# Kernel optimization log

Hardware: AMD Instinct MI355X
Metric: run time of the kernel (lower is better)

Reference implementation:

```python
import jax, jax.numpy as jnp
import numpy as np

K = 128   # per-head dim == input dim
H = 8     # heads
B = 2
T = 2048


def setup_inputs() -> dict:
    key = jax.random.key(0)
    ks = jax.random.split(key, 6)
    s_in = 1.0 / np.sqrt(K)
    s_out = 1.0 / np.sqrt(K * H)
    return {
        "x": jax.random.normal(ks[0], (B, T, K), dtype=jnp.float32),
        # Linear weights stored as (in, out); torch Linear init ~ U(-1/sqrt(in), 1/sqrt(in))
        "Wq": jax.random.uniform(ks[1], (K, K * H), jnp.float32, -s_in, s_in),
        "Wk": jax.random.uniform(ks[2], (K, K * H), jnp.float32, -s_in, s_in),
        "Wv": jax.random.uniform(ks[3], (K, K * H), jnp.float32, -s_in, s_in),
        "Wo": jax.random.uniform(ks[4], (K * H, K), jnp.float32, -s_out, s_out),
        "bo": jax.random.uniform(ks[5], (K,), jnp.float32, -s_out, s_out),
    }


def reference(x, Wq, Wk, Wv, Wo, bo):
    b, t, k = x.shape
    h = H
    scale = k ** 0.25
    # projections -> [b, t, h, k]
    q = (x @ Wq).reshape(b, t, h, k) / scale
    ke = (x @ Wk).reshape(b, t, h, k) / scale
    v = (x @ Wv).reshape(b, t, h, k)
    # scores: [b, h, t, t]
    scores = jnp.einsum('bihk,bjhk->bhij', q, ke)
    # causal mask: positions j > i get -inf (diagonal kept)
    causal = jnp.tril(jnp.ones((t, t), dtype=bool))
    scores = jnp.where(causal[None, None], scores, -jnp.inf)
    p = jax.nn.softmax(scores, axis=-1)
    out = jnp.einsum('bhij,bjhk->bihk', p, v).reshape(b, t, h * k)
    return out @ Wo + bo
```

## Files before the change

kernel.cpp:

```cpp
#include <hip/hip_runtime.h>

typedef __bf16 bf16;
typedef __bf16 bf16x4 __attribute__((ext_vector_type(4)));
typedef __bf16 bf16x8 __attribute__((ext_vector_type(8)));
typedef float f32x4 __attribute__((ext_vector_type(4)));
typedef float f32x16 __attribute__((ext_vector_type(16)));
typedef int i32x4 __attribute__((ext_vector_type(4)));

#define MFMA16(a, b, c) __builtin_amdgcn_mfma_f32_16x16x32_bf16((a), (b), (c), 0, 0, 0)
#define MFMA32(a, b, c) __builtin_amdgcn_mfma_f32_32x32x16_bf16((a), (b), (c), 0, 0, 0)

__device__ __forceinline__ int swz16(int r, int c) { return (c ^ (r & 15)); }

__device__ __forceinline__ int cvt_pk_bf16(float lo, float hi) {
  int r;
  asm("v_cvt_pk_bf16_f32 %0, %1, %2" : "=v"(r) : "v"(lo), "v"(hi));
  return r;
}

__global__ __launch_bounds__(256) void trW_kernel(
    const float* __restrict__ Wq, const float* __restrict__ Wk,
    const float* __restrict__ Wv, const float* __restrict__ Wo,
    bf16* __restrict__ outbase) {
  __shared__ bf16 tile[32][33];
  const int z = blockIdx.z;
  const float* ib = (z == 0) ? Wq : (z == 1) ? Wk : (z == 2) ? Wv : Wo;
  bf16* ob = outbase + (size_t)z * 131072;
  const int R = (z < 3) ? 128 : 1024;
  const int C = (z < 3) ? 1024 : 128;
  int r0 = (z < 3) ? blockIdx.y * 32 : blockIdx.x * 32;
  int c0 = (z < 3) ? blockIdx.x * 32 : blockIdx.y * 32;
  int tx = threadIdx.x & 31, ty = threadIdx.x >> 5;
#pragma unroll
  for (int i = 0; i < 4; ++i) {
    int r = ty + i * 8;
    tile[r][tx] = (bf16)ib[(size_t)(r0 + r) * C + (c0 + tx)];
  }
  __syncthreads();
#pragma unroll
  for (int i = 0; i < 4; ++i) {
    int r = ty + i * 8;
    ob[(size_t)(c0 + r) * R + (r0 + tx)] = tile[tx][r];
  }
}

__global__ __launch_bounds__(256) void proj_gemm(
    const float* __restrict__ x, const bf16* __restrict__ Wqt,
    const bf16* __restrict__ Wkt, const bf16* __restrict__ Wvt,
    bf16* __restrict__ Qf, bf16* __restrict__ Kf, bf16* __restrict__ Vf) {
  __shared__ __align__(16) bf16 As[128 * 128];
  __shared__ __align__(16) bf16 Bs[128 * 128];
  const int mt = blockIdx.x;
  const int nt = blockIdx.y;
  const int matid = nt >> 3, h = nt & 7;
  const bf16* W = (matid == 0) ? Wqt : (matid == 1) ? Wkt : Wvt;
  const int tid = threadIdx.x;
  const bf16* sb = W + (size_t)h * 128 * 128;
#pragma unroll
  for (int i = 0; i < 8; ++i) {
    int c = tid + i * 256;
    int r = c >> 4, cc = c & 15;
    const f32x4* p = (const f32x4*)(x + (size_t)(mt * 128 + r) * 128 + cc * 8);
    f32x4 a = p[0], b = p[1];
    bf16x8 o;
#pragma unroll
    for (int j = 0; j < 4; ++j) { o[j] = (bf16)a[j]; o[4 + j] = (bf16)b[j]; }
    *(bf16x8*)&As[r * 128 + swz16(r, cc) * 8] = o;
  }
#pragma unroll
  for (int i = 0; i < 8; ++i) {
    int c = tid + i * 256;
    int r = c >> 4, cc = c & 15;
    *(bf16x8*)&Bs[r * 128 + swz16(r, cc) * 8] = *(const bf16x8*)(sb + (size_t)r * 128 + cc * 8);
  }
  __syncthreads();
  const int wave = tid >> 6, lane = tid & 63;
  const int wr = (wave >> 1) * 64, wc = (wave & 1) * 64;
  const int lr = lane & 15, lkb = lane >> 4;
  const f32x4 FZ = {0.f, 0.f, 0.f, 0.f};
  f32x4 acc[4][4];
#pragma unroll
  for (int mf = 0; mf < 4; ++mf)
#pragma unroll
    for (int nf = 0; nf < 4; ++nf) acc[mf][nf] = FZ;
  const bool qk = (matid < 2);
#pragma unroll
  for (int ks = 0; ks < 4; ++ks) {
    bf16x8 a[4], b[4];
#pragma unroll
    for (int mf = 0; mf < 4; ++mf) {
      int r = wr + mf * 16 + lr;
      a[mf] = *(const bf16x8*)&As[r * 128 + swz16(r, ks * 4 + lkb) * 8];
    }
#pragma unroll
    for (int nf = 0; nf < 4; ++nf) {
      int r = wc + nf * 16 + lr;
      b[nf] = *(const bf16x8*)&Bs[r * 128 + swz16(r, ks * 4 + lkb) * 8];
    }
    if (qk) {
#pragma unroll
      for (int mf = 0; mf < 4; ++mf)
#pragma unroll
        for (int nf = 0; nf < 4; ++nf) acc[mf][nf] = MFMA16(b[nf], a[mf], acc[mf][nf]);
    } else {
#pragma unroll
      for (int mf = 0; mf < 4; ++mf)
#pragma unroll
        for (int nf = 0; nf < 4; ++nf) acc[mf][nf] = MFMA16(a[mf], b[nf], acc[mf][nf]);
    }
  }
  const int rb = lkb * 4;
  if (qk) {
    bf16* Out = (matid == 0) ? Qf : Kf;
#pragma unroll
    for (int mf = 0; mf < 4; ++mf)
#pragma unroll
      for (int nf = 0; nf < 4; ++nf) {
        int m = mt * 128 + wr + mf * 16 + lr;
        int d0 = wc + nf * 16 + rb;
        int bb = m >> 11, t = m & 2047;
        bf16x4 vv;
#pragma unroll
        for (int r = 0; r < 4; ++r) vv[r] = (bf16)acc[mf][nf][r];
        size_t e = (size_t)(bb * 8 + h) * 262144
                 + (size_t)(((t >> 5) * 8 + (d0 >> 4)) * 512 + ((d0 >> 3) & 1) * 256
                            + (t & 31) * 8 + (d0 & 7));
        *(bf16x4*)(Out + e) = vv;
      }
  } else {
#pragma unroll
    for (int mf = 0; mf < 4; ++mf)
#pragma unroll
      for (int nf = 0; nf < 4; ++nf) {
        int d = wc + nf * 16 + lr;
        int m0 = mt * 128 + wr + mf * 16 + rb;
        int bb = m0 >> 11, t0 = m0 & 2047;
        bf16x4 vv;
#pragma unroll
        for (int r = 0; r < 4; ++r) vv[r] = (bf16)acc[mf][nf][r];
        size_t e = (size_t)(bb * 8 + h) * 262144
                 + (size_t)((d >> 5) * 65536 + (t0 >> 4) * 512 + ((t0 >> 3) & 1) * 256
                            + (d & 31) * 8 + (t0 & 7));
        *(bf16x4*)(Vf + e) = vv;
      }
  }
}

__global__ __launch_bounds__(256, 3) void attn_kernel(
    bf16* __restrict__ Qf, const bf16* __restrict__ Kf, const bf16* __restrict__ Vf) {
  __shared__ float Om0[128 * 32];
  __shared__ float Om1[128 * 32];
  __shared__ float L0m[32], L0l[32], L1m[32], L1l[32];
  const int bid = blockIdx.x;
  const int bh = bid & 15;
  const int qt = 63 - (bid >> 4);
  const int tid = threadIdx.x;
  const int w = tid >> 6, lane = tid & 63;
  const int lq = lane & 31, hi = lane >> 5;
  const int lo = hi * 256 + lq * 8;
  const bf16* Qh = Qf + (size_t)bh * 262144;
  const bf16* Kh = Kf + (size_t)bh * 262144;
  const bf16* Vh = Vf + (size_t)bh * 262144;
  const float SCL = 0.12751744f;

  const int nT = (qt >> 1) + 1;
  const int base = nT >> 2, rem = nT & 3;
  const int cnt = base + (w < rem ? 1 : 0);
  const int tb = w * base + (w < rem ? w : rem);

  bf16x8 qf[8];
#pragma unroll
  for (int ks = 0; ks < 8; ++ks)
    qf[ks] = *(const bf16x8*)(Qh + qt * 4096 + ks * 512 + lo);

  float mrun = -__builtin_inff(), lrun = 0.f;
  f32x16 O[4];
#pragma unroll
  for (int dt = 0; dt < 4; ++dt)
#pragma unroll
    for (int r = 0; r < 16; ++r) O[dt][r] = 0.f;

  for (int it = 0; it < cnt; ++it) {
    const int kvt = tb + it;
    const int kv0 = kvt * 64;
    const bf16* kbase = Kh + kvt * 8192 + lo;
    bf16x8 ka[8], kb[8];
#pragma unroll
    for (int i = 0; i < 8; ++i) ka[i] = *(const bf16x8*)(kbase + i * 512);
#pragma unroll
    for (int i = 0; i < 8; ++i) kb[i] = *(const bf16x8*)(kbase + 4096 + i * 512);
    f32x16 p0, p1;
#pragma unroll
    for (int r = 0; r < 16; ++r) { p0[r] = 0.f; p1[r] = 0.f; }
    __builtin_amdgcn_s_setprio(1);
#pragma unroll
    for (int ks = 0; ks < 8; ++ks) p0 = MFMA32(ka[ks], qf[ks], p0);
#pragma unroll
    for (int ks = 0; ks < 8; ++ks) p1 = MFMA32(kb[ks], qf[ks], p1);
    __builtin_amdgcn_s_setprio(0);
    const bf16* vbase = Vh + kvt * 2048 + lo;
    bf16x8 va[8];
#pragma unroll
    for (int i = 0; i < 8; ++i)
      va[i] = *(const bf16x8*)(vbase + (i >> 2) * 65536 + (i & 3) * 512);
    if (kvt == (qt >> 1)) {
      const int qg = qt * 32 + lq;
#pragma unroll
      for (int r = 0; r < 16; ++r) {
        int kvr = kv0 + (r & 3) + 8 * (r >> 2) + 4 * hi;
        if (kvr > qg) p0[r] = -__builtin_inff();
        if (kvr + 32 > qg) p1[r] = -__builtin_inff();
      }
    }
    float m0 = fmaxf(p0[0], p1[0]);
    float m1_ = fmaxf(p0[1], p1[1]);
    float m2 = fmaxf(p0[2], p1[2]);
    float m3 = fmaxf(p0[3], p1[3]);
#pragma unroll
    for (int r = 4; r < 16; r += 4) {
      m0 = fmaxf(m0, fmaxf(p0[r], p1[r]));
      m1_ = fmaxf(m1_, fmaxf(p0[r + 1], p1[r + 1]));
      m2 = fmaxf(m2, fmaxf(p0[r + 2], p1[r + 2]));
      m3 = fmaxf(m3, fmaxf(p0[r + 3], p1[r + 3]));
    }
    float pm = fmaxf(fmaxf(m0, m1_), fmaxf(m2, m3));
    pm = fmaxf(pm, __shfl_xor(pm, 32, 64));
    float pmS = pm * SCL;
    if (!__all(pmS <= mrun + 8.f)) {
      float mnew = fmaxf(mrun, pmS);
      float alpha = exp2f(mrun - mnew);
      mrun = mnew;
      lrun *= alpha;
#pragma unroll
      for (int dt = 0; dt < 4; ++dt)
#pragma unroll
        for (int r = 0; r < 16; ++r) O[dt][r] *= alpha;
    }
    float s0 = 0.f, s1 = 0.f, s2 = 0.f, s3 = 0.f;
#pragma unroll
    for (int r = 0; r < 16; r += 4) {
      float a0_ = exp2f(__builtin_fmaf(p0[r], SCL, -mrun));
      float a1_ = exp2f(__builtin_fmaf(p0[r + 1], SCL, -mrun));
      float a2_ = exp2f(__builtin_fmaf(p0[r + 2], SCL, -mrun));
      float a3_ = exp2f(__builtin_fmaf(p0[r + 3], SCL, -mrun));
      float b0_ = exp2f(__builtin_fmaf(p1[r], SCL, -mrun));
      float b1_ = exp2f(__builtin_fmaf(p1[r + 1], SCL, -mrun));
      float b2_ = exp2f(__builtin_fmaf(p1[r + 2], SCL, -mrun));
      float b3_ = exp2f(__builtin_fmaf(p1[r + 3], SCL, -mrun));
      p0[r] = a0_; p0[r + 1] = a1_; p0[r + 2] = a2_; p0[r + 3] = a3_;
      p1[r] = b0_; p1[r + 1] = b1_; p1[r + 2] = b2_; p1[r + 3] = b3_;
      s0 += a0_ + b0_; s1 += a1_ + b1_; s2 += a2_ + b2_; s3 += a3_ + b3_;
    }
    float ps = (s0 + s1) + (s2 + s3);
    ps += __shfl_xor(ps, 32, 64);
    lrun += ps;
    int wd[16];
#pragma unroll
    for (int i = 0; i < 8; ++i) wd[i] = cvt_pk_bf16(p0[2 * i], p0[2 * i + 1]);
#pragma unroll
    for (int i = 0; i < 8; ++i) wd[8 + i] = cvt_pk_bf16(p1[2 * i], p1[2 * i + 1]);
    bf16x8 pa[4];
#pragma unroll
    for (int t4 = 0; t4 < 4; ++t4) {
      int b0 = t4 * 4;
      int e0 = __shfl_xor(wd[b0 + 0], 32, 64);
      int e1 = __shfl_xor(wd[b0 + 1], 32, 64);
      int e2 = __shfl_xor(wd[b0 + 2], 32, 64);
      int e3 = __shfl_xor(wd[b0 + 3], 32, 64);
      i32x4 f;
      f[0] = hi ? e2 : wd[b0 + 0];
      f[1] = hi ? e3 : wd[b0 + 1];
      f[2] = hi ? wd[b0 + 2] : e0;
      f[3] = hi ? wd[b0 + 3] : e1;
      pa[t4] = __builtin_bit_cast(bf16x8, f);
    }
    bf16x8 vb[8];
#pragma unroll
    for (int i = 0; i < 8; ++i)
      vb[i] = *(const bf16x8*)(vbase + 131072 + (i >> 2) * 65536 + (i & 3) * 512);
    __builtin_amdgcn_s_setprio(1);
#pragma unroll
    for (int dt = 0; dt < 2; ++dt) {
      O[dt] = MFMA32(va[dt * 4 + 0], pa[0], O[dt]);
      O[dt] = MFMA32(va[dt * 4 + 1], pa[1], O[dt]);
      O[dt] = MFMA32(va[dt * 4 + 2], pa[2], O[dt]);
      O[dt] = MFMA32(va[dt * 4 + 3], pa[3], O[dt]);
    }
#pragma unroll
    for (int dt = 0; dt < 2; ++dt) {
      O[2 + dt] = MFMA32(vb[dt * 4 + 0], pa[0], O[2 + dt]);
      O[2 + dt] = MFMA32(vb[dt * 4 + 1], pa[1], O[2 + dt]);
      O[2 + dt] = MFMA32(vb[dt * 4 + 2], pa[2], O[2 + dt]);
      O[2 + dt] = MFMA32(vb[dt * 4 + 3], pa[3], O[2 + dt]);
    }
    __builtin_amdgcn_s_setprio(0);
  }

  auto STORE = [&](float* Om, float* Lm, float* Ll) {
#pragma unroll
    for (int dt = 0; dt < 4; ++dt)
#pragma unroll
      for (int r = 0; r < 16; ++r)
        Om[(dt * 32 + (r & 3) + 8 * (r >> 2) + 4 * hi) * 32 + lq] = O[dt][r];
    if (!hi) { Lm[lq] = mrun; Ll[lq] = lrun; }
  };
  auto MERGE = [&](const float* Om, const float* Lm, const float* Ll) {
    float m1 = Lm[lq], l1 = Ll[lq];
    float mF = fmaxf(mrun, m1);
    float a0 = (mrun < -3.0e38f) ? 0.f : exp2f(mrun - mF);
    float a1 = (m1 < -3.0e38f) ? 0.f : exp2f(m1 - mF);
    lrun = lrun * a0 + l1 * a1;
#pragma unroll
    for (int dt = 0; dt < 4; ++dt)
#pragma unroll
      for (int r = 0; r < 16; ++r)
        O[dt][r] = O[dt][r] * a0 +
                   Om[(dt * 32 + (r & 3) + 8 * (r >> 2) + 4 * hi) * 32 + lq] * a1;
    mrun = mF;
  };

  if (w == 1) STORE(Om0, L0m, L0l);
  if (w == 3) STORE(Om1, L1m, L1l);
  __syncthreads();
  if (w == 0) MERGE(Om0, L0m, L0l);
  if (w == 2) MERGE(Om1, L1m, L1l);
  __syncthreads();
  if (w == 2) STORE(Om0, L0m, L0l);
  __syncthreads();
  if (w == 0) {
    MERGE(Om0, L0m, L0l);
    float inv = 1.f / lrun;
    bf16* qw = Qf + (size_t)bh * 262144 + qt * 4096 + lq * 8 + 4 * hi;
#pragma unroll
    for (int dt = 0; dt < 4; ++dt) {
#pragma unroll
      for (int rq = 0; rq < 4; ++rq) {
        bf16x4 vv;
#pragma unroll
        for (int jj = 0; jj < 4; ++jj) {
          int r = rq * 4 + jj;
          vv[jj] = (bf16)(O[dt][r] * inv);
        }
        *(bf16x4*)(qw + (dt * 2 + (rq >> 1)) * 512 + (rq & 1) * 256) = vv;
      }
    }
  }
}

__global__ __launch_bounds__(256) void outproj_kernel(
    const bf16* __restrict__ AO, const bf16* __restrict__ Wot,
    const float* __restrict__ bo, float* __restrict__ out) {
  __shared__ __align__(16) bf16 As[16 * 128];
  __shared__ __align__(16) bf16 Bs[128 * 128];
  const f32x4 FZ = {0.f, 0.f, 0.f, 0.f};
  const int mt = blockIdx.x;
  const int tid = threadIdx.x, wave = tid >> 6, lane = tid & 63;
  const int lr = lane & 15, lkb = lane >> 4, rb = lkb * 4;
  const int wc = wave * 32;
  f32x4 acc[2];
  acc[0] = FZ; acc[1] = FZ;
  for (int kt = 0; kt < 8; ++kt) {
    __syncthreads();
    {
      int r = tid >> 4, cc = tid & 15;
      int m = mt * 16 + r, bb = m >> 11, t = m & 2047;
      const bf16* src = AO + (size_t)(bb * 8 + kt) * 262144
          + ((t >> 5) * 8 + (cc >> 1)) * 512 + (cc & 1) * 256 + (t & 31) * 8;
      *(bf16x8*)&As[r * 128 + swz16(r, cc) * 8] = *(const bf16x8*)src;
    }
#pragma unroll
    for (int i = 0; i < 8; ++i) {
      int c = tid + i * 256;
      int r = c >> 4, cc = c & 15;
      *(bf16x8*)&Bs[r * 128 + swz16(r, cc) * 8] =
          *(const bf16x8*)(Wot + (size_t)r * 1024 + kt * 128 + cc * 8);
    }
    __syncthreads();
#pragma unroll
    for (int ks = 0; ks < 4; ++ks) {
      bf16x8 a = *(const bf16x8*)&As[lr * 128 + swz16(lr, ks * 4 + lkb) * 8];
#pragma unroll
      for (int nf = 0; nf < 2; ++nf) {
        int r = wc + nf * 16 + lr;
        bf16x8 b = *(const bf16x8*)&Bs[r * 128 + swz16(r, ks * 4 + lkb) * 8];
        acc[nf] = MFMA16(a, b, acc[nf]);
      }
    }
  }
#pragma unroll
  for (int nf = 0; nf < 2; ++nf)
#pragma unroll
    for (int r = 0; r < 4; ++r) {
      int m = mt * 16 + rb + r;
      int n = wc + nf * 16 + lr;
      out[(size_t)m * 128 + n] = acc[nf][r] + bo[n];
    }
}

extern "C" void kernel_launch(void* const* d_in, const int* in_sizes, int n_in,
                              void* d_out, int out_size, void* d_ws, size_t ws_size,
                              hipStream_t stream) {
  (void)in_sizes; (void)n_in; (void)out_size; (void)ws_size;
  const float* x  = (const float*)d_in[0];
  const float* Wq = (const float*)d_in[1];
  const float* Wk = (const float*)d_in[2];
  const float* Wv = (const float*)d_in[3];
  const float* Wo = (const float*)d_in[4];
  const float* bo = (const float*)d_in[5];
  float* out = (float*)d_out;

  bf16* ws  = (bf16*)d_ws;
  bf16* Wqt = ws;
  bf16* Wkt = Wqt + 131072;
  bf16* Wvt = Wkt + 131072;
  bf16* Wot = Wvt + 131072;
  bf16* Qf  = Wot + 131072;
  bf16* Kf  = Qf + 4194304;
  bf16* Vf  = Kf + 4194304;

  trW_kernel<<<dim3(32, 4, 4), 256, 0, stream>>>(Wq, Wk, Wv, Wo, Wqt);
  proj_gemm<<<dim3(32, 24, 1), 256, 0, stream>>>(x, Wqt, Wkt, Wvt, Qf, Kf, Vf);
  attn_kernel<<<dim3(1024, 1, 1), 256, 0, stream>>>(Qf, Kf, Vf);
  outproj_kernel<<<dim3(256, 1, 1), 256, 0, stream>>>(Qf, Wot, bo, out);
}
```

Baseline: 160.7 us.

## Pair causal q-tiles per block with 512-thread blocks for balanced attention work

Restructures the attention kernel so each 512-thread block handles two adjacent 32-row query tiles, with two groups of four waves, and processes two phases pairing query tile pr with 31-pr. This balances causal work per block and shrinks the grid from 1024 to 256 blocks, each with a 66.5KB dynamic-shared-memory merge buffer. It also shares K/V tiles between the two query groups in cache. The 256-block grid and large LDS footprint limit occupancy to about one block per CU, and the extra barriers between phases add synchronisation cost.

```diff
diff --git a/kernel.cpp b/kernel.cpp
--- a/kernel.cpp
+++ b/kernel.cpp
@@ -146,16 +146,16 @@
   }
 }
 
-__global__ __launch_bounds__(256, 3) void attn_kernel(
+__global__ __launch_bounds__(512) void attn_kernel(
     bf16* __restrict__ Qf, const bf16* __restrict__ Kf, const bf16* __restrict__ Vf) {
-  __shared__ float Om0[128 * 32];
-  __shared__ float Om1[128 * 32];
-  __shared__ float L0m[32], L0l[32], L1m[32], L1l[32];
+  extern __shared__ char smem[];
   const int bid = blockIdx.x;
   const int bh = bid & 15;
-  const int qt = 63 - (bid >> 4);
+  const int pr = bid >> 4;
   const int tid = threadIdx.x;
   const int w = tid >> 6, lane = tid & 63;
+  const int qs = w >> 2;
+  const int k4 = w & 3;
   const int lq = lane & 31, hi = lane >> 5;
   const int lo = hi * 256 + lq * 8;
   const bf16* Qh = Qf + (size_t)bh * 262144;
@@ -163,185 +163,202 @@
   const bf16* Vh = Vf + (size_t)bh * 262144;
   const float SCL = 0.12751744f;
 
-  const int nT = (qt >> 1) + 1;
-  const int base = nT >> 2, rem = nT & 3;
-  const int cnt = base + (w < rem ? 1 : 0);
-  const int tb = w * base + (w < rem ? w : rem);
-
-  bf16x8 qf[8];
-#pragma unroll
-  for (int ks = 0; ks < 8; ++ks)
-    qf[ks] = *(const bf16x8*)(Qh + qt * 4096 + ks * 512 + lo);
-
-  float mrun = -__builtin_inff(), lrun = 0.f;
-  f32x16 O[4];
-#pragma unroll
-  for (int dt = 0; dt < 4; ++dt)
-#pragma unroll
-    for (int r = 0; r < 16; ++r) O[dt][r] = 0.f;
-
-  for (int it = 0; it < cnt; ++it) {
-    const int kvt = tb + it;
-    const int kv0 = kvt * 64;
-    const bf16* kbase = Kh + kvt * 8192 + lo;
-    bf16x8 ka[8], kb[8];
-#pragma unroll
-    for (int i = 0; i < 8; ++i) ka[i] = *(const bf16x8*)(kbase + i * 512);
-#pragma unroll
-    for (int i = 0; i < 8; ++i) kb[i] = *(const bf16x8*)(kbase + 4096 + i * 512);
-    f32x16 p0, p1;
-#pragma unroll
-    for (int r = 0; r < 16; ++r) { p0[r] = 0.f; p1[r] = 0.f; }
-    __builtin_amdgcn_s_setprio(1);
-#pragma unroll
-    for (int ks = 0; ks < 8; ++ks) p0 = MFMA32(ka[ks], qf[ks], p0);
-#pragma unroll
-    for (int ks = 0; ks < 8; ++ks) p1 = MFMA32(kb[ks], qf[ks], p1);
-    __builtin_amdgcn_s_setprio(0);
-    const bf16* vbase = Vh + kvt * 2048 + lo;
-    bf16x8 va[8];
-#pragma unroll
-    for (int i = 0; i < 8; ++i)
-      va[i] = *(const bf16x8*)(vbase + (i >> 2) * 65536 + (i & 3) * 512);
-    if (kvt == (qt >> 1)) {
-      const int qg = qt * 32 + lq;
-#pragma unroll
-      for (int r = 0; r < 16; ++r) {
-        int kvr = kv0 + (r & 3) + 8 * (r >> 2) + 4 * hi;
-        if (kvr > qg) p0[r] = -__builtin_inff();
-        if (kvr + 32 > qg) p1[r] = -__builtin_inff();
-      }
-    }
-    float m0 = fmaxf(p0[0], p1[0]);
-    float m1_ = fmaxf(p0[1], p1[1]);
-    float m2 = fmaxf(p0[2], p1[2]);
-    float m3 = fmaxf(p0[3], p1[3]);
-#pragma unroll
-    for (int r = 4; r < 16; r += 4) {
-      m0 = fmaxf(m0, fmaxf(p0[r], p1[r]));
-      m1_ = fmaxf(m1_, fmaxf(p0[r + 1], p1[r + 1]));
-      m2 = fmaxf(m2, fmaxf(p0[r + 2], p1[r + 2]));
-      m3 = fmaxf(m3, fmaxf(p0[r + 3], p1[r + 3]));
-    }
-    float pm = fmaxf(fmaxf(m0, m1_), fmaxf(m2, m3));
-    pm = fmaxf(pm, __shfl_xor(pm, 32, 64));
-    float pmS = pm * SCL;
-    if (!__all(pmS <= mrun + 8.f)) {
-      float mnew = fmaxf(mrun, pmS);
-      float alpha = exp2f(mrun - mnew);
-      mrun = mnew;
-      lrun *= alpha;
+  float* OmB[4];
+  float* LmB[4];
+  float* LlB[4];
+#pragma unroll
+  for (int b = 0; b < 4; ++b) {
+    OmB[b] = (float*)(smem + b * 16384);
+    LmB[b] = (float*)(smem + 65536 + b * 128);
+    LlB[b] = (float*)(smem + 66048 + b * 128);
+  }
+
+  for (int ph = 0; ph < 2; ++ph) {
+    const int qt64 = ph ? (31 - pr) : pr;
+    const int nT = qt64 + 1;
+    const int qblk = qt64 * 2 + qs;
+    const int k4e = ph ? (3 - k4) : k4;
+    const int base = nT >> 2, rem = nT & 3;
+    const int cnt = base + (k4e < rem ? 1 : 0);
+    const int tb = k4e * base + (k4e < rem ? k4e : rem);
+
+    bf16x8 qf[8];
+#pragma unroll
+    for (int ks = 0; ks < 8; ++ks)
+      qf[ks] = *(const bf16x8*)(Qh + qblk * 4096 + ks * 512 + lo);
+
+    float mrun = -__builtin_inff(), lrun = 0.f;
+    f32x16 O[4];
+#pragma unroll
+    for (int dt = 0; dt < 4; ++dt)
+#pragma unroll
+      for (int r = 0; r < 16; ++r) O[dt][r] = 0.f;
+
+    for (int it = 0; it < cnt; ++it) {
+      const int kvt = tb + it;
+      const int kv0 = kvt * 64;
+      const bf16* kbase = Kh + kvt * 8192 + lo;
+      bf16x8 ka[8], kb[8];
+#pragma unroll
+      for (int i = 0; i < 8; ++i) ka[i] = *(const bf16x8*)(kbase + i * 512);
+#pragma unroll
+      for (int i = 0; i < 8; ++i) kb[i] = *(const bf16x8*)(kbase + 4096 + i * 512);
+      f32x16 p0, p1;
+#pragma unroll
+      for (int r = 0; r < 16; ++r) { p0[r] = 0.f; p1[r] = 0.f; }
+      __builtin_amdgcn_s_setprio(1);
+#pragma unroll
+      for (int ks = 0; ks < 8; ++ks) p0 = MFMA32(ka[ks], qf[ks], p0);
+#pragma unroll
+      for (int ks = 0; ks < 8; ++ks) p1 = MFMA32(kb[ks], qf[ks], p1);
+      __builtin_amdgcn_s_setprio(0);
+      const bf16* vbase = Vh + kvt * 2048 + lo;
+      bf16x8 va[8];
+#pragma unroll
+      for (int i = 0; i < 8; ++i)
+        va[i] = *(const bf16x8*)(vbase + (i >> 2) * 65536 + (i & 3) * 512);
+      if (kvt == qt64) {
+        const int qg = qblk * 32 + lq;
+#pragma unroll
+        for (int r = 0; r < 16; ++r) {
+          int kvr = kv0 + (r & 3) + 8 * (r >> 2) + 4 * hi;
+          if (kvr > qg) p0[r] = -__builtin_inff();
+          if (kvr + 32 > qg) p1[r] = -__builtin_inff();
+        }
+      }
+      float m0 = fmaxf(p0[0], p1[0]);
+      float m1_ = fmaxf(p0[1], p1[1]);
+      float m2 = fmaxf(p0[2], p1[2]);
+      float m3 = fmaxf(p0[3], p1[3]);
+#pragma unroll
+      for (int r = 4; r < 16; r += 4) {
+        m0 = fmaxf(m0, fmaxf(p0[r], p1[r]));
+        m1_ = fmaxf(m1_, fmaxf(p0[r + 1], p1[r + 1]));
+        m2 = fmaxf(m2, fmaxf(p0[r + 2], p1[r + 2]));
+        m3 = fmaxf(m3, fmaxf(p0[r + 3], p1[r + 3]));
+      }
+      float pm = fmaxf(fmaxf(m0, m1_), fmaxf(m2, m3));
+      pm = fmaxf(pm, __shfl_xor(pm, 32, 64));
+      float pmS = pm * SCL;
+      if (!__all(pmS <= mrun + 8.f)) {
+        float mnew = fmaxf(mrun, pmS);
+        float alpha = exp2f(mrun - mnew);
+        mrun = mnew;
+        lrun *= alpha;
+#pragma unroll
+        for (int dt = 0; dt < 4; ++dt)
+#pragma unroll
+          for (int r = 0; r < 16; ++r) O[dt][r] *= alpha;
+      }
+      float s0 = 0.f, s1 = 0.f, s2 = 0.f, s3 = 0.f;
+#pragma unroll
+      for (int r = 0; r < 16; r += 4) {
+        float a0_ = exp2f(__builtin_fmaf(p0[r], SCL, -mrun));
+        float a1_ = exp2f(__builtin_fmaf(p0[r + 1], SCL, -mrun));
+        float a2_ = exp2f(__builtin_fmaf(p0[r + 2], SCL, -mrun));
+        float a3_ = exp2f(__builtin_fmaf(p0[r + 3], SCL, -mrun));
+        float b0_ = exp2f(__builtin_fmaf(p1[r], SCL, -mrun));
+        float b1_ = exp2f(__builtin_fmaf(p1[r + 1], SCL, -mrun));
+        float b2_ = exp2f(__builtin_fmaf(p1[r + 2], SCL, -mrun));
+        float b3_ = exp2f(__builtin_fmaf(p1[r + 3], SCL, -mrun));
+        p0[r] = a0_; p0[r + 1] = a1_; p0[r + 2] = a2_; p0[r + 3] = a3_;
+        p1[r] = b0_; p1[r + 1] = b1_; p1[r + 2] = b2_; p1[r + 3] = b3_;
+        s0 += a0_ + b0_; s1 += a1_ + b1_; s2 += a2_ + b2_; s3 += a3_ + b3_;
+      }
+      float ps = (s0 + s1) + (s2 + s3);
+      ps += __shfl_xor(ps, 32, 64);
+      lrun += ps;
+      int wd[16];
+#pragma unroll
+      for (int i = 0; i < 8; ++i) wd[i] = cvt_pk_bf16(p0[2 * i], p0[2 * i + 1]);
+#pragma unroll
+      for (int i = 0; i < 8; ++i) wd[8 + i] = cvt_pk_bf16(p1[2 * i], p1[2 * i + 1]);
+      bf16x8 pa[4];
+#pragma unroll
+      for (int t4 = 0; t4 < 4; ++t4) {
+        int b0 = t4 * 4;
+        int e0 = __shfl_xor(wd[b0 + 0], 32, 64);
+        int e1 = __shfl_xor(wd[b0 + 1], 32, 64);
+        int e2 = __shfl_xor(wd[b0 + 2], 32, 64);
+        int e3 = __shfl_xor(wd[b0 + 3], 32, 64);
+        i32x4 f;
+        f[0] = hi ? e2 : wd[b0 + 0];
+        f[1] = hi ? e3 : wd[b0 + 1];
+        f[2] = hi ? wd[b0 + 2] : e0;
+        f[3] = hi ? wd[b0 + 3] : e1;
+        pa[t4] = __builtin_bit_cast(bf16x8, f);
+      }
+      bf16x8 vb[8];
+#pragma unroll
+      for (int i = 0; i < 8; ++i)
+        vb[i] = *(const bf16x8*)(vbase + 131072 + (i >> 2) * 65536 + (i & 3) * 512);
+      __builtin_amdgcn_s_setprio(1);
+#pragma unroll
+      for (int dt = 0; dt < 2; ++dt) {
+        O[dt] = MFMA32(va[dt * 4 + 0], pa[0], O[dt]);
+        O[dt] = MFMA32(va[dt * 4 + 1], pa[1], O[dt]);
+        O[dt] = MFMA32(va[dt * 4 + 2], pa[2], O[dt]);
+        O[dt] = MFMA32(va[dt * 4 + 3], pa[3], O[dt]);
+      }
+#pragma unroll
+      for (int dt = 0; dt < 2; ++dt) {
+        O[2 + dt] = MFMA32(vb[dt * 4 + 0], pa[0], O[2 + dt]);
+        O[2 + dt] = MFMA32(vb[dt * 4 + 1], pa[1], O[2 + dt]);
+        O[2 + dt] = MFMA32(vb[dt * 4 + 2], pa[2], O[2 + dt]);
+        O[2 + dt] = MFMA32(vb[dt * 4 + 3], pa[3], O[2 + dt]);
+      }
+      __builtin_amdgcn_s_setprio(0);
+    }
+
+    auto STORE = [&](float* Om, float* Lm, float* Ll) {
 #pragma unroll
       for (int dt = 0; dt < 4; ++dt)
 #pragma unroll
-        for (int r = 0; r < 16; ++r) O[dt][r] *= alpha;
-    }
-    float s0 = 0.f, s1 = 0.f, s2 = 0.f, s3 = 0.f;
-#pragma unroll
-    for (int r = 0; r < 16; r += 4) {
-      float a0_ = exp2f(__builtin_fmaf(p0[r], SCL, -mrun));
-      float a1_ = exp2f(__builtin_fmaf(p0[r + 1], SCL, -mrun));
-      float a2_ = exp2f(__builtin_fmaf(p0[r + 2], SCL, -mrun));
-      float a3_ = exp2f(__builtin_fmaf(p0[r + 3], SCL, -mrun));
-      float b0_ = exp2f(__builtin_fmaf(p1[r], SCL, -mrun));
-      float b1_ = exp2f(__builtin_fmaf(p1[r + 1], SCL, -mrun));
-      float b2_ = exp2f(__builtin_fmaf(p1[r + 2], SCL, -mrun));
-      float b3_ = exp2f(__builtin_fmaf(p1[r + 3], SCL, -mrun));
-      p0[r] = a0_; p0[r + 1] = a1_; p0[r + 2] = a2_; p0[r + 3] = a3_;
-      p1[r] = b0_; p1[r + 1] = b1_; p1[r + 2] = b2_; p1[r + 3] = b3_;
-      s0 += a0_ + b0_; s1 += a1_ + b1_; s2 += a2_ + b2_; s3 += a3_ + b3_;
-    }
-    float ps = (s0 + s1) + (s2 + s3);
-    ps += __shfl_xor(ps, 32, 64);
-    lrun += ps;
-    int wd[16];
-#pragma unroll
-    for (int i = 0; i < 8; ++i) wd[i] = cvt_pk_bf16(p0[2 * i], p0[2 * i + 1]);
-#pragma unroll
-    for (int i = 0; i < 8; ++i) wd[8 + i] = cvt_pk_bf16(p1[2 * i], p1[2 * i + 1]);
-    bf16x8 pa[4];
-#pragma unroll
-    for (int t4 = 0; t4 < 4; ++t4) {
-      int b0 = t4 * 4;
-      int e0 = __shfl_xor(wd[b0 + 0], 32, 64);
-      int e1 = __shfl_xor(wd[b0 + 1], 32, 64);
-      int e2 = __shfl_xor(wd[b0 + 2], 32, 64);
-      int e3 = __shfl_xor(wd[b0 + 3], 32, 64);
-      i32x4 f;
-      f[0] = hi ? e2 : wd[b0 + 0];
-      f[1] = hi ? e3 : wd[b0 + 1];
-      f[2] = hi ? wd[b0 + 2] : e0;
-      f[3] = hi ? wd[b0 + 3] : e1;
-      pa[t4] = __builtin_bit_cast(bf16x8, f);
-    }
-    bf16x8 vb[8];
-#pragma unroll
-    for (int i = 0; i < 8; ++i)
-      vb[i] = *(const bf16x8*)(vbase + 131072 + (i >> 2) * 65536 + (i & 3) * 512);
-    __builtin_amdgcn_s_setprio(1);
-#pragma unroll
-    for (int dt = 0; dt < 2; ++dt) {
-      O[dt] = MFMA32(va[dt * 4 + 0], pa[0], O[dt]);
-      O[dt] = MFMA32(va[dt * 4 + 1], pa[1], O[dt]);
-      O[dt] = MFMA32(va[dt * 4 + 2], pa[2], O[dt]);
-      O[dt] = MFMA32(va[dt * 4 + 3], pa[3], O[dt]);
-    }
-#pragma unroll
-    for (int dt = 0; dt < 2; ++dt) {
-      O[2 + dt] = MFMA32(vb[dt * 4 + 0], pa[0], O[2 + dt]);
-      O[2 + dt] = MFMA32(vb[dt * 4 + 1], pa[1], O[2 + dt]);
-      O[2 + dt] = MFMA32(vb[dt * 4 + 2], pa[2], O[2 + dt]);
-      O[2 + dt] = MFMA32(vb[dt * 4 + 3], pa[3], O[2 + dt]);
-    }
-    __builtin_amdgcn_s_setprio(0);
-  }
-
-  auto STORE = [&](float* Om, float* Lm, float* Ll) {
-#pragma unroll
-    for (int dt = 0; dt < 4; ++dt)
-#pragma unroll
-      for (int r = 0; r < 16; ++r)
-        Om[(dt * 32 + (r & 3) + 8 * (r >> 2) + 4 * hi) * 32 + lq] = O[dt][r];
-    if (!hi) { Lm[lq] = mrun; Ll[lq] = lrun; }
-  };
-  auto MERGE = [&](const float* Om, const float* Lm, const float* Ll) {
-    float m1 = Lm[lq], l1 = Ll[lq];
-    float mF = fmaxf(mrun, m1);
-    float a0 = (mrun < -3.0e38f) ? 0.f : exp2f(mrun - mF);
-    float a1 = (m1 < -3.0e38f) ? 0.f : exp2f(m1 - mF);
-    lrun = lrun * a0 + l1 * a1;
-#pragma unroll
-    for (int dt = 0; dt < 4; ++dt)
-#pragma unroll
-      for (int r = 0; r < 16; ++r)
-        O[dt][r] = O[dt][r] * a0 +
-                   Om[(dt * 32 + (r & 3) + 8 * (r >> 2) + 4 * hi) * 32 + lq] * a1;
-    mrun = mF;
-  };
-
-  if (w == 1) STORE(Om0, L0m, L0l);
-  if (w == 3) STORE(Om1, L1m, L1l);
-  __syncthreads();
-  if (w == 0) MERGE(Om0, L0m, L0l);
-  if (w == 2) MERGE(Om1, L1m, L1l);
-  __syncthreads();
-  if (w == 2) STORE(Om0, L0m, L0l);
-  __syncthreads();
-  if (w == 0) {
-    MERGE(Om0, L0m, L0l);
-    float inv = 1.f / lrun;
-    bf16* qw = Qf + (size_t)bh * 262144 + qt * 4096 + lq * 8 + 4 * hi;
-#pragma unroll
-    for (int dt = 0; dt < 4; ++dt) {
-#pragma unroll
-      for (int rq = 0; rq < 4; ++rq) {
-        bf16x4 vv;
-#pragma unroll
-        for (int jj = 0; jj < 4; ++jj) {
-          int r = rq * 4 + jj;
-          vv[jj] = (bf16)(O[dt][r] * inv);
+        for (int r = 0; r < 16; ++r)
+          Om[(dt * 32 + (r & 3) + 8 * (r >> 2) + 4 * hi) * 32 + lq] = O[dt][r];
+      if (!hi) { Lm[lq] = mrun; Ll[lq] = lrun; }
+    };
+    auto MERGE = [&](const float* Om, const float* Lm, const float* Ll) {
+      float m1 = Lm[lq], l1 = Ll[lq];
+      float mF = fmaxf(mrun, m1);
+      float a0 = (mrun < -3.0e38f) ? 0.f : exp2f(mrun - mF);
+      float a1 = (m1 < -3.0e38f) ? 0.f : exp2f(m1 - mF);
+      lrun = lrun * a0 + l1 * a1;
+#pragma unroll
+      for (int dt = 0; dt < 4; ++dt)
+#pragma unroll
+        for (int r = 0; r < 16; ++r)
+          O[dt][r] = O[dt][r] * a0 +
+                     Om[(dt * 32 + (r & 3) + 8 * (r >> 2) + 4 * hi) * 32 + lq] * a1;
+      mrun = mF;
+    };
+
+    const int bA = qs * 2, bB = qs * 2 + 1;
+    __syncthreads();
+    if (k4 == 1) STORE(OmB[bA], LmB[bA], LlB[bA]);
+    if (k4 == 3) STORE(OmB[bB], LmB[bB], LlB[bB]);
+    __syncthreads();
+    if (k4 == 0) MERGE(OmB[bA], LmB[bA], LlB[bA]);
+    if (k4 == 2) MERGE(OmB[bB], LmB[bB], LlB[bB]);
+    __syncthreads();
+    if (k4 == 2) STORE(OmB[bA], LmB[bA], LlB[bA]);
+    __syncthreads();
+    if (k4 == 0) {
+      MERGE(OmB[bA], LmB[bA], LlB[bA]);
+      float inv = 1.f / lrun;
+      bf16* qw = Qf + (size_t)bh * 262144 + qblk * 4096 + lq * 8 + 4 * hi;
+#pragma unroll
+      for (int dt = 0; dt < 4; ++dt) {
+#pragma unroll
+        for (int rq = 0; rq < 4; ++rq) {
+          bf16x4 vv;
+#pragma unroll
+          for (int jj = 0; jj < 4; ++jj) {
+            int r = rq * 4 + jj;
+            vv[jj] = (bf16)(O[dt][r] * inv);
+          }
+          *(bf16x4*)(qw + (dt * 2 + (rq >> 1)) * 512 + (rq & 1) * 256) = vv;
         }
-        *(bf16x4*)(qw + (dt * 2 + (rq >> 1)) * 512 + (rq & 1) * 256) = vv;
       }
     }
   }
@@ -420,6 +437,6 @@
 
   trW_kernel<<<dim3(32, 4, 4), 256, 0, stream>>>(Wq, Wk, Wv, Wo, Wqt);
   proj_gemm<<<dim3(32, 24, 1), 256, 0, stream>>>(x, Wqt, Wkt, Wvt, Qf, Kf, Vf);
-  attn_kernel<<<dim3(1024, 1, 1), 256, 0, stream>>>(Qf, Kf, Vf);
+  attn_kernel<<<dim3(256, 1, 1), 512, 66560, stream>>>(Qf, Kf, Vf);
   outproj_kernel<<<dim3(256, 1, 1), 256, 0, stream>>>(Qf, Wot, bo, out);
 }
```

New measurement: 229.0 us. +42.5%, slower.
